# Optimization experiments

Measured on AMD Instinct MI355X. Metric: run time of the kernel, lower is better.

## Reference

```python
import jax, jax.numpy as jnp
import numpy as np

N = 50000       # nodes
E = 500000      # edges
F_IN = 64       # input feature dim
F_OUT = 64      # hidden/output dim
K = 3           # diffusion filter order
C = F_IN + F_OUT  # concat dim seen by each DConv


def _xavier(k, shape):
    fan_in, fan_out = shape[-2], shape[-1]
    lim = float(np.sqrt(6.0 / (fan_in + fan_out)))
    return jax.random.uniform(k, shape, jnp.float32, -lim, lim)


def setup_inputs() -> dict:
    key = jax.random.key(0)
    ks = jax.random.split(key, 8)
    X = jax.random.normal(ks[0], (N, F_IN), jnp.float32)
    H = jax.random.normal(ks[1], (N, F_OUT), jnp.float32)
    # ring edges guarantee every node has in-degree >= 1 and out-degree >= 1
    base = jnp.arange(N, dtype=jnp.int32)
    row = jnp.concatenate([base, jax.random.randint(ks[2], (E - N,), 0, N, jnp.int32)])
    col = jnp.concatenate([jnp.roll(base, 1), jax.random.randint(ks[3], (E - N,), 0, N, jnp.int32)])
    edge_index = jnp.stack([row, col])  # [2, E]
    W_z = _xavier(ks[4], (2, K, C, F_OUT))
    W_r = _xavier(ks[5], (2, K, C, F_OUT))
    W_h = _xavier(ks[6], (2, K, C, F_OUT))
    b = jnp.zeros((F_OUT,), jnp.float32)
    return {"X": X, "edge_index": edge_index, "H": H,
            "W_z": W_z, "b_z": b, "W_r": W_r, "b_r": b, "W_h": W_h, "b_h": b}


def _dconv(Xc, row, col, norm_out, norm_in, W, b):
    # PyG propagate: gather source (row) features, scale by edge norm, scatter-add to target (col)
    def prop(x, norm):
        return jax.ops.segment_sum(norm[:, None] * x[row], col, num_segments=N)
    Tx_0 = Xc
    Hout = Xc @ (W[0, 0] + W[1, 0])
    Tx_1_o = prop(Xc, norm_out)
    Tx_1_i = prop(Xc, norm_in)
    Hout = Hout + Tx_1_o @ W[0, 1] + Tx_1_i @ W[1, 1]
    for k in range(2, K):
        Tx_2_o = 2.0 * prop(Tx_1_o, norm_out) - Tx_0
        Tx_2_i = 2.0 * prop(Tx_1_i, norm_in) - Tx_0
        Hout = Hout + Tx_2_o @ W[0, k] + Tx_2_i @ W[1, k]
        # faithful to original: Tx_1 is never reassigned, so Tx_0 stays Xc
        Tx_0, Tx_1_o, Tx_1_i = Xc, Tx_2_o, Tx_2_i
    return Hout + b


def reference(X, edge_index, H, W_z, b_z, W_r, b_r, W_h, b_h):
    row, col = edge_index[0], edge_index[1]
    deg_out = jnp.zeros((N,), jnp.float32).at[row].add(1.0)
    deg_in = jnp.zeros((N,), jnp.float32).at[col].add(1.0)
    norm_out = (1.0 / deg_out)[row]
    norm_in = (1.0 / deg_in)[row]
    XH = jnp.concatenate([X, H], axis=1)
    Z = jax.nn.sigmoid(_dconv(XH, row, col, norm_out, norm_in, W_z, b_z))
    R = jax.nn.sigmoid(_dconv(XH, row, col, norm_out, norm_in, W_r, b_r))
    XHR = jnp.concatenate([X, H * R], axis=1)
    H_tilde = jnp.tanh(_dconv(XHR, row, col, norm_out, norm_in, W_h, b_h))
    H_new = Z * H + (1.0 - Z) * H_tilde
    # NaN infill with mean of non-NaN entries (faithful to original)
    mask = jnp.isnan(H_new)
    H_new = jnp.where(mask, jnp.nanmean(H_new), H_new)
    return H_new
```

## Files before the change

kernel.cpp:

```cpp
#include <hip/hip_runtime.h>
#include <hip/hip_bf16.h>
#include <math.h>

#define N_NODES 50000
#define N_EDGES 500000
#define C_DIM 128

typedef __attribute__((ext_vector_type(8))) short bf8;
typedef __attribute__((ext_vector_type(4))) float f32x4;

__device__ __forceinline__ float bflo(unsigned u) { return __uint_as_float(u << 16); }
__device__ __forceinline__ float bfhi(unsigned u) { return __uint_as_float(u & 0xffff0000u); }
__device__ __forceinline__ unsigned short f2bfu(float f) {
    __hip_bfloat16 h = __float2bfloat16(f);
    unsigned short u;
    __builtin_memcpy(&u, &h, 2);
    return u;
}
__device__ __forceinline__ unsigned packbf(float a, float b) {
    return ((unsigned)f2bfu(b) << 16) | f2bfu(a);
}


__global__ void count_deg(const int* __restrict__ row, const int* __restrict__ col,
                          int* __restrict__ dout, int* __restrict__ din, int e) {
    int i = blockIdx.x * blockDim.x + threadIdx.x;
    if (i >= e) return;
    atomicAdd(&dout[row[i]], 1);
    atomicAdd(&din[col[i]], 1);
}

__global__ void scan_block(const int* __restrict__ counts, int* __restrict__ excl,
                           int* __restrict__ blocksums, int n) {
    __shared__ int tmp[1024];
    int tid = threadIdx.x;
    int gid = blockIdx.x * 1024 + tid;
    int v = (gid < n) ? counts[gid] : 0;
    tmp[tid] = v;
    __syncthreads();
    for (int off = 1; off < 1024; off <<= 1) {
        int t = (tid >= off) ? tmp[tid - off] : 0;
        __syncthreads();
        tmp[tid] += t;
        __syncthreads();
    }
    int incl = tmp[tid];
    if (gid < n) excl[gid] = incl - v;
    if (tid == 1023) blocksums[blockIdx.x] = incl;
}

__global__ void scan_sums(int* __restrict__ blocksums, int nb) {
    __shared__ int tmp[64];
    int tid = threadIdx.x;
    int v = (tid < nb) ? blocksums[tid] : 0;
    tmp[tid] = v;
    __syncthreads();
    for (int off = 1; off < 64; off <<= 1) {
        int t = (tid >= off) ? tmp[tid - off] : 0;
        __syncthreads();
        tmp[tid] += t;
        __syncthreads();
    }
    if (tid < nb) blocksums[tid] = tmp[tid] - v;
}

__global__ void scan_add(int* __restrict__ rowptr, const int* __restrict__ blocksums,
                         int* __restrict__ cursor, const int* __restrict__ dout,
                         const int* __restrict__ din, float2* __restrict__ winv,
                         int n, int e_total) {
    int gid = blockIdx.x * blockDim.x + threadIdx.x;
    if (gid < n) {
        int v = rowptr[gid] + blocksums[gid >> 10];
        rowptr[gid] = v;
        cursor[gid] = v;
        winv[gid] = make_float2(1.0f / (float)dout[gid], 1.0f / (float)din[gid]);
    }
    if (gid == n) rowptr[n] = e_total;
}

__global__ void build_csr(const int* __restrict__ row, const int* __restrict__ col,
                          const float2* __restrict__ winv,
                          int* __restrict__ cursor, int* __restrict__ src,
                          float2* __restrict__ w, int e) {
    int i = blockIdx.x * blockDim.x + threadIdx.x;
    if (i >= e) return;
    int r = row[i], c = col[i];
    int pos = atomicAdd(&cursor[c], 1);
    src[pos] = r;
    w[pos] = winv[r];
}

__device__ __forceinline__ float wraw(const float* W, int d, int kk, int k, int j) {
    return W[((d * 3 + kk) * 128 + k) * 64 + j];
}

__global__ void pack_weights(const float* __restrict__ Wz, const float* __restrict__ Wr,
                             const float* __restrict__ Wh,
                             unsigned short* __restrict__ Wzr_t,
                             unsigned short* __restrict__ Wh_t) {
    int i = blockIdx.x * blockDim.x + threadIdx.x;
    if (i < 128 * 640) {
        int k = i % 640;
        int nn = i / 640;
        const float* W = (nn < 64) ? Wz : Wr;
        int j = nn & 63;
        float v;
        if (k < 128) {
            v = wraw(W, 0, 0, k, j) + wraw(W, 1, 0, k, j);
        } else {
            int k2 = k - 128;
            int kk = (k2 >= 256) ? 2 : 1;
            int k3 = k2 & 255;
            int p = k3 >> 2, sub = k3 & 3;
            v = wraw(W, sub >> 1, kk, 2 * p + (sub & 1), j);
        }
        Wzr_t[i] = f2bfu(v);
    } else if (i < 128 * 640 + 64 * 640) {
        int i2 = i - 128 * 640;
        int k = i2 % 640;
        int j = i2 / 640;
        float v;
        if (k < 64) {
            v = wraw(Wh, 0, 0, k, j) + wraw(Wh, 1, 0, k, j);
        } else if (k < 320) {
            int k2 = k - 64;
            int kk = (k2 >= 128) ? 2 : 1;
            int k3 = k2 & 127;
            int p = k3 >> 2, sub = k3 & 3;
            v = wraw(Wh, sub >> 1, kk, 2 * p + (sub & 1), j);
        } else if (k < 384) {
            int rr = k - 320;
            v = wraw(Wh, 0, 0, 64 + rr, j) + wraw(Wh, 1, 0, 64 + rr, j);
        } else {
            int k2 = k - 384;
            int kk = (k2 >= 128) ? 2 : 1;
            int k3 = k2 & 127;
            int p = k3 >> 2, sub = k3 & 3;
            v = wraw(Wh, sub >> 1, kk, 64 + 2 * p + (sub & 1), j);
        }
        Wh_t[i2] = f2bfu(v);
    }
}


__global__ void concat_xh(const float* __restrict__ X, const float* __restrict__ H,
                          unsigned short* __restrict__ XH, int n) {
    int i = blockIdx.x * blockDim.x + threadIdx.x;
    if (i >= n * C_DIM) return;
    int r = i >> 7, c = i & 127;
    float v = (c < 64) ? X[r * 64 + c] : H[r * 64 + (c - 64)];
    XH[i] = f2bfu(v);
}


__global__ void prop1_128(const unsigned short* __restrict__ S,
                          const int* __restrict__ rowptr, const int* __restrict__ src,
                          const float2* __restrict__ w,
                          unsigned short* __restrict__ P1, int n) {
    int tid = blockIdx.x * blockDim.x + threadIdx.x;
    int lane = tid & 63;
    int node = ((tid >> 6) << 1) + (lane >> 5);
    int p = lane & 31;
    if (node >= n) return;
    int beg = rowptr[node], end = rowptr[node + 1];
    float ao0 = 0.f, ao1 = 0.f, ao2 = 0.f, ao3 = 0.f;
    float ai0 = 0.f, ai1 = 0.f, ai2 = 0.f, ai3 = 0.f;
    int j = beg;
#define P1STEP(s_, w_) {                                                     \
        uint2 u = *(const uint2*)(S + (size_t)(s_) * 128 + 4 * p);           \
        float c0 = bflo(u.x), c1 = bfhi(u.x), c2 = bflo(u.y), c3 = bfhi(u.y);\
        ao0 = fmaf(w_.x, c0, ao0); ao1 = fmaf(w_.x, c1, ao1);                \
        ao2 = fmaf(w_.x, c2, ao2); ao3 = fmaf(w_.x, c3, ao3);                \
        ai0 = fmaf(w_.y, c0, ai0); ai1 = fmaf(w_.y, c1, ai1);                \
        ai2 = fmaf(w_.y, c2, ai2); ai3 = fmaf(w_.y, c3, ai3); }
    for (; j + 4 <= end; j += 4) {
        int s0 = src[j], s1 = src[j + 1], s2 = src[j + 2], s3 = src[j + 3];
        float2 w0 = w[j], w1 = w[j + 1], w2 = w[j + 2], w3 = w[j + 3];
        P1STEP(s0, w0); P1STEP(s1, w1); P1STEP(s2, w2); P1STEP(s3, w3);
    }
    for (; j < end; ++j) {
        int s = src[j]; float2 wv = w[j];
        P1STEP(s, wv);
    }
#undef P1STEP
    uint4 o;
    o.x = packbf(ao0, ao1); o.y = packbf(ai0, ai1);
    o.z = packbf(ao2, ao3); o.w = packbf(ai2, ai3);
    *(uint4*)(P1 + (size_t)node * 256 + 8 * p) = o;
}

__global__ void prop2_128(const unsigned short* __restrict__ P1,
                          const unsigned short* __restrict__ Xc,
                          const int* __restrict__ rowptr, const int* __restrict__ src,
                          const float2* __restrict__ w,
                          unsigned short* __restrict__ P2, int n) {
    int tid = blockIdx.x * blockDim.x + threadIdx.x;
    int lane = tid & 63;
    int node = ((tid >> 6) << 1) + (lane >> 5);
    int p = lane & 31;
    if (node >= n) return;
    int beg = rowptr[node], end = rowptr[node + 1];
    float oa = 0.f, ob = 0.f, oc = 0.f, od = 0.f;
    float ia = 0.f, ib = 0.f, ic = 0.f, id = 0.f;
    int j = beg;
#define P2STEP(s_, w_) {                                                     \
        uint4 v = *(const uint4*)(P1 + (size_t)(s_) * 256 + 8 * p);          \
        oa = fmaf(w_.x, bflo(v.x), oa); ob = fmaf(w_.x, bfhi(v.x), ob);      \
        ia = fmaf(w_.y, bflo(v.y), ia); ib = fmaf(w_.y, bfhi(v.y), ib);      \
        oc = fmaf(w_.x, bflo(v.z), oc); od = fmaf(w_.x, bfhi(v.z), od);      \
        ic = fmaf(w_.y, bflo(v.w), ic); id = fmaf(w_.y, bfhi(v.w), id); }
    for (; j + 4 <= end; j += 4) {
        int s0 = src[j], s1 = src[j + 1], s2 = src[j + 2], s3 = src[j + 3];
        float2 w0 = w[j], w1 = w[j + 1], w2 = w[j + 2], w3 = w[j + 3];
        P2STEP(s0, w0); P2STEP(s1, w1); P2STEP(s2, w2); P2STEP(s3, w3);
    }
    for (; j < end; ++j) {
        int s = src[j]; float2 wv = w[j];
        P2STEP(s, wv);
    }
#undef P2STEP
    uint2 ux = *(const uint2*)(Xc + (size_t)node * 128 + 4 * p);
    float xa = bflo(ux.x), xb = bfhi(ux.x), xc = bflo(ux.y), xd = bfhi(ux.y);
    uint4 o;
    o.x = packbf(2.f * oa - xa, 2.f * ob - xb);
    o.y = packbf(2.f * ia - xa, 2.f * ib - xb);
    o.z = packbf(2.f * oc - xc, 2.f * od - xd);
    o.w = packbf(2.f * ic - xc, 2.f * id - xd);
    *(uint4*)(P2 + (size_t)node * 256 + 8 * p) = o;
}

__global__ void prop1_64(const unsigned short* __restrict__ HR,
                         const int* __restrict__ rowptr, const int* __restrict__ src,
                         const float2* __restrict__ w,
                         unsigned short* __restrict__ Q1, int n) {
    int tid = blockIdx.x * blockDim.x + threadIdx.x;
    int lane = tid & 63;
    int node = ((tid >> 6) << 2) + (lane >> 4);
    int p = lane & 15;
    if (node >= n) return;
    int beg = rowptr[node], end = rowptr[node + 1];
    float ao0 = 0.f, ao1 = 0.f, ao2 = 0.f, ao3 = 0.f;
    float ai0 = 0.f, ai1 = 0.f, ai2 = 0.f, ai3 = 0.f;
    int j = beg;
#define Q1STEP(s_, w_) {                                                     \
        uint2 u = *(const uint2*)(HR + (size_t)(s_) * 64 + 4 * p);           \
        float c0 = bflo(u.x), c1 = bfhi(u.x), c2 = bflo(u.y), c3 = bfhi(u.y);\
        ao0 = fmaf(w_.x, c0, ao0); ao1 = fmaf(w_.x, c1, ao1);                \
        ao2 = fmaf(w_.x, c2, ao2); ao3 = fmaf(w_.x, c3, ao3);                \
        ai0 = fmaf(w_.y, c0, ai0); ai1 = fmaf(w_.y, c1, ai1);                \
        ai2 = fmaf(w_.y, c2, ai2); ai3 = fmaf(w_.y, c3, ai3); }
    for (; j + 4 <= end; j += 4) {
        int s0 = src[j], s1 = src[j + 1], s2 = src[j + 2], s3 = src[j + 3];
        float2 w0 = w[j], w1 = w[j + 1], w2 = w[j + 2], w3 = w[j + 3];
        Q1STEP(s0, w0); Q1STEP(s1, w1); Q1STEP(s2, w2); Q1STEP(s3, w3);
    }
    for (; j < end; ++j) {
        int s = src[j]; float2 wv = w[j];
        Q1STEP(s, wv);
    }
#undef Q1STEP
    uint4 o;
    o.x = packbf(ao0, ao1); o.y = packbf(ai0, ai1);
    o.z = packbf(ao2, ao3); o.w = packbf(ai2, ai3);
    *(uint4*)(Q1 + (size_t)node * 128 + 8 * p) = o;
}

__global__ void prop2_64(const unsigned short* __restrict__ Q1,
                         const unsigned short* __restrict__ HR,
                         const int* __restrict__ rowptr, const int* __restrict__ src,
                         const float2* __restrict__ w,
                         unsigned short* __restrict__ Q2, int n) {
    int tid = blockIdx.x * blockDim.x + threadIdx.x;
    int lane = tid & 63;
    int node = ((tid >> 6) << 2) + (lane >> 4);
    int p = lane & 15;
    if (node >= n) return;
    int beg = rowptr[node], end = rowptr[node + 1];
    float oa = 0.f, ob = 0.f, oc = 0.f, od = 0.f;
    float ia = 0.f, ib = 0.f, ic = 0.f, id = 0.f;
    int j = beg;
#define Q2STEP(s_, w_) {                                                     \
        uint4 v = *(const uint4*)(Q1 + (size_t)(s_) * 128 + 8 * p);          \
        oa = fmaf(w_.x, bflo(v.x), oa); ob = fmaf(w_.x, bfhi(v.x), ob);      \
        ia = fmaf(w_.y, bflo(v.y), ia); ib = fmaf(w_.y, bfhi(v.y), ib);      \
        oc = fmaf(w_.x, bflo(v.z), oc); od = fmaf(w_.x, bfhi(v.z), od);      \
        ic = fmaf(w_.y, bflo(v.w), ic); id = fmaf(w_.y, bfhi(v.w), id); }
    for (; j + 4 <= end; j += 4) {
        int s0 = src[j], s1 = src[j + 1], s2 = src[j + 2], s3 = src[j + 3];
        float2 w0 = w[j], w1 = w[j + 1], w2 = w[j + 2], w3 = w[j + 3];
        Q2STEP(s0, w0); Q2STEP(s1, w1); Q2STEP(s2, w2); Q2STEP(s3, w3);
    }
    for (; j < end; ++j) {
        int s = src[j]; float2 wv = w[j];
        Q2STEP(s, wv);
    }
#undef Q2STEP
    uint2 ux = *(const uint2*)(HR + (size_t)node * 64 + 4 * p);
    float xa = bflo(ux.x), xb = bfhi(ux.x), xc = bflo(ux.y), xd = bfhi(ux.y);
    uint4 o;
    o.x = packbf(2.f * oa - xa, 2.f * ob - xb);
    o.y = packbf(2.f * ia - xa, 2.f * ib - xb);
    o.z = packbf(2.f * oc - xc, 2.f * od - xd);
    o.w = packbf(2.f * ic - xc, 2.f * id - xd);
    *(uint4*)(Q2 + (size_t)node * 128 + 8 * p) = o;
}


__global__ __launch_bounds__(256) void gemm_zr_mfma(
    const unsigned short* __restrict__ XH, const unsigned short* __restrict__ P1,
    const unsigned short* __restrict__ P2,
    const unsigned short* __restrict__ Wt, const float* __restrict__ bz,
    const float* __restrict__ br, const float* __restrict__ H,
    float* __restrict__ Zf, unsigned short* __restrict__ HR, int n) {
    __shared__ uint2 Wl[128 * 66];
    int tid = threadIdx.x;
    int lane = tid & 63;
    int wid = tid >> 6;
    int mhalf = wid & 1, nhalf = wid >> 1;
    int rowbase = blockIdx.x * 64 + mhalf * 32;
    int lr = lane & 15, quad = lane >> 4;
    int r0 = rowbase + lr;       if (r0 >= n) r0 = n - 1;
    int r1 = rowbase + 16 + lr;  if (r1 >= n) r1 = n - 1;

    f32x4 zero = {0.f, 0.f, 0.f, 0.f};
    f32x4 acc[2][4];
#pragma unroll
    for (int a = 0; a < 2; ++a)
#pragma unroll
        for (int b = 0; b < 4; ++b) acc[a][b] = zero;

    const unsigned short* Ab[5] = {XH, P1, P1, P2, P2};
    const int Astr[5] = {128, 256, 256, 256, 256};
    const int Aoff[5] = {0, 0, 128, 0, 128};

    for (int c = 0; c < 5; ++c) {
        const unsigned short* Wsrc = Wt + c * 128;
        for (int i = tid; i < 128 * 16; i += 256) {
            int nrow = i >> 4, kp = i & 15;
            uint4 v = *(const uint4*)(Wsrc + (size_t)nrow * 640 + kp * 8);
            *(uint4*)&Wl[nrow * 66 + kp * 2] = v;
        }
        __syncthreads();
        const unsigned short* A0 = Ab[c] + (size_t)r0 * Astr[c] + Aoff[c] + quad * 8;
        const unsigned short* A1 = Ab[c] + (size_t)r1 * Astr[c] + Aoff[c] + quad * 8;
#pragma unroll
        for (int kk = 0; kk < 4; ++kk) {
            bf8 a0 = *(const bf8*)(A0 + kk * 32);
            bf8 a1 = *(const bf8*)(A1 + kk * 32);
#pragma unroll
            for (int nt = 0; nt < 4; ++nt) {
                int nrow = nhalf * 64 + nt * 16 + lr;
                int base = nrow * 66 + kk * 8 + quad * 2;
                union { bf8 v; uint2 h[2]; } bb;
                bb.h[0] = Wl[base];
                bb.h[1] = Wl[base + 1];
                acc[0][nt] = __builtin_amdgcn_mfma_f32_16x16x32_bf16(a0, bb.v, acc[0][nt], 0, 0, 0);
                acc[1][nt] = __builtin_amdgcn_mfma_f32_16x16x32_bf16(a1, bb.v, acc[1][nt], 0, 0, 0);
            }
        }
        __syncthreads();
    }
#pragma unroll
    for (int mt = 0; mt < 2; ++mt)
#pragma unroll
        for (int reg = 0; reg < 4; ++reg) {
            int r = rowbase + mt * 16 + quad * 4 + reg;
            if (r >= n) continue;
#pragma unroll
            for (int nt = 0; nt < 4; ++nt) {
                int cidx = nhalf * 64 + nt * 16 + lr;
                float bias = (cidx < 64) ? bz[cidx] : br[cidx - 64];
                float v = acc[mt][nt][reg] + bias;
                float s = 1.f / (1.f + expf(-v));
                if (cidx < 64) {
                    Zf[(size_t)r * 64 + cidx] = s;
                } else {
                    int c2 = cidx - 64;
                    HR[(size_t)r * 64 + c2] = f2bfu(H[(size_t)r * 64 + c2] * s);
                }
            }
        }
}

__global__ __launch_bounds__(256) void gemm_h_mfma(
    const unsigned short* __restrict__ XH, const unsigned short* __restrict__ P1,
    const unsigned short* __restrict__ P2, const unsigned short* __restrict__ HR,
    const unsigned short* __restrict__ Q1, const unsigned short* __restrict__ Q2,
    const unsigned short* __restrict__ Wt, const float* __restrict__ bh,
    const float* __restrict__ Zf, const float* __restrict__ H,
    float* __restrict__ out, int n) {
    __shared__ uint2 Wl[64 * 66];
    int tid = threadIdx.x;
    int lane = tid & 63;
    int wid = tid >> 6;
    int mhalf = wid & 1, nhalf = wid >> 1;
    int rowbase = blockIdx.x * 64 + mhalf * 32;
    int lr = lane & 15, quad = lane >> 4;
    int r0 = rowbase + lr;       if (r0 >= n) r0 = n - 1;
    int r1 = rowbase + 16 + lr;  if (r1 >= n) r1 = n - 1;

    f32x4 zero = {0.f, 0.f, 0.f, 0.f};
    f32x4 acc[2][2];
#pragma unroll
    for (int a = 0; a < 2; ++a)
#pragma unroll
        for (int b = 0; b < 2; ++b) acc[a][b] = zero;

    const unsigned short* Ab[6] = {XH, P1, P2, HR, Q1, Q2};
    const int Astr[6] = {128, 256, 256, 64, 128, 128};
    const int Aklen[6] = {64, 128, 128, 64, 128, 128};
    const int Akg[6] = {0, 64, 192, 320, 384, 512};

    for (int sg = 0; sg < 6; ++sg) {
        int klen = Aklen[sg];
        int units = 64 * (klen >> 3);
        const unsigned short* Wsrc = Wt + Akg[sg];
        for (int i = tid; i < units; i += 256) {
            int kcnt = klen >> 3;
            int nrow = i / kcnt, kp = i % kcnt;
            uint4 v = *(const uint4*)(Wsrc + (size_t)nrow * 640 + kp * 8);
            *(uint4*)&Wl[nrow * 66 + kp * 2] = v;
        }
        __syncthreads();
        const unsigned short* A0 = Ab[sg] + (size_t)r0 * Astr[sg] + quad * 8;
        const unsigned short* A1 = Ab[sg] + (size_t)r1 * Astr[sg] + quad * 8;
        int nkk = klen >> 5;
        for (int kk = 0; kk < nkk; ++kk) {
            bf8 a0 = *(const bf8*)(A0 + kk * 32);
            bf8 a1 = *(const bf8*)(A1 + kk * 32);
#pragma unroll
            for (int nt = 0; nt < 2; ++nt) {
                int nrow = nhalf * 32 + nt * 16 + lr;
                int base = nrow * 66 + kk * 8 + quad * 2;
                union { bf8 v; uint2 h[2]; } bb;
                bb.h[0] = Wl[base];
                bb.h[1] = Wl[base + 1];
                acc[0][nt] = __builtin_amdgcn_mfma_f32_16x16x32_bf16(a0, bb.v, acc[0][nt], 0, 0, 0);
                acc[1][nt] = __builtin_amdgcn_mfma_f32_16x16x32_bf16(a1, bb.v, acc[1][nt], 0, 0, 0);
            }
        }
        __syncthreads();
    }
#pragma unroll
    for (int mt = 0; mt < 2; ++mt)
#pragma unroll
        for (int reg = 0; reg < 4; ++reg) {
            int r = rowbase + mt * 16 + quad * 4 + reg;
            if (r >= n) continue;
#pragma unroll
            for (int nt = 0; nt < 2; ++nt) {
                int cidx = nhalf * 32 + nt * 16 + lr;
                float ht = tanhf(acc[mt][nt][reg] + bh[cidx]);
                float z = Zf[(size_t)r * 64 + cidx];
                float h_old = H[(size_t)r * 64 + cidx];
                out[(size_t)r * 64 + cidx] = z * h_old + (1.f - z) * ht;
            }
        }
}


static inline size_t rup(size_t x) { return (x + 63) & ~(size_t)63; }

extern "C" void kernel_launch(void* const* d_in, const int* in_sizes, int n_in,
                              void* d_out, int out_size, void* d_ws, size_t ws_size,
                              hipStream_t stream) {
    const float* X  = (const float*)d_in[0];
    const int*   EI = (const int*)d_in[1];
    const float* H  = (const float*)d_in[2];
    const float* Wz = (const float*)d_in[3];
    const float* bz = (const float*)d_in[4];
    const float* Wr = (const float*)d_in[5];
    const float* br = (const float*)d_in[6];
    const float* Wh = (const float*)d_in[7];
    const float* bh = (const float*)d_in[8];
    float* out = (float*)d_out;

    const int* row = EI;
    const int* col = EI + N_EDGES;

    char* ws = (char*)d_ws;
    size_t off = 0;
    auto carve = [&](size_t bytes) { void* p = ws + off; off += rup(bytes); return p; };

    int*   deg_out   = (int*)carve(N_NODES * 4);
    int*   deg_in    = (int*)carve(N_NODES * 4);
    int*   rowptr    = (int*)carve((N_NODES + 1) * 4);
    int*   cursor    = (int*)carve(N_NODES * 4);
    int*   blocksums = (int*)carve(64 * 4);
    float2* winv     = (float2*)carve(N_NODES * 8);
    int*   csr_src   = (int*)carve(N_EDGES * 4);
    float2* csr_w    = (float2*)carve(N_EDGES * 8);
    unsigned short* XH = (unsigned short*)carve((size_t)N_NODES * 128 * 2);
    unsigned short* P1 = (unsigned short*)carve((size_t)N_NODES * 256 * 2);
    unsigned short* P2 = (unsigned short*)carve((size_t)N_NODES * 256 * 2);
    unsigned short* HR = (unsigned short*)carve((size_t)N_NODES * 64 * 2);
    unsigned short* Q1 = (unsigned short*)carve((size_t)N_NODES * 128 * 2);
    unsigned short* Q2 = (unsigned short*)carve((size_t)N_NODES * 128 * 2);
    float* Zf          = (float*)carve((size_t)N_NODES * 64 * 4);
    unsigned short* Wzr_t = (unsigned short*)carve(128 * 640 * 2);
    unsigned short* Wh_t  = (unsigned short*)carve(64 * 640 * 2);

    hipMemsetAsync(deg_out, 0, rup(N_NODES * 4) + rup(N_NODES * 4), stream);
    count_deg<<<(N_EDGES + 255) / 256, 256, 0, stream>>>(row, col, deg_out, deg_in, N_EDGES);

    int nblk = (N_NODES + 1023) / 1024;
    scan_block<<<nblk, 1024, 0, stream>>>(deg_in, rowptr, blocksums, N_NODES);
    scan_sums<<<1, 64, 0, stream>>>(blocksums, nblk);
    scan_add<<<(N_NODES + 1 + 255) / 256, 256, 0, stream>>>(rowptr, blocksums, cursor,
                                                            deg_out, deg_in, winv, N_NODES, N_EDGES);

    build_csr<<<(N_EDGES + 255) / 256, 256, 0, stream>>>(row, col, winv, cursor,
                                                         csr_src, csr_w, N_EDGES);

    pack_weights<<<(128 * 640 + 64 * 640 + 255) / 256, 256, 0, stream>>>(Wz, Wr, Wh, Wzr_t, Wh_t);

    concat_xh<<<(N_NODES * C_DIM + 255) / 256, 256, 0, stream>>>(X, H, XH, N_NODES);

    int blocks_p128 = (((N_NODES + 1) / 2) * 64 + 255) / 256;
    prop1_128<<<blocks_p128, 256, 0, stream>>>(XH, rowptr, csr_src, csr_w, P1, N_NODES);
    prop2_128<<<blocks_p128, 256, 0, stream>>>(P1, XH, rowptr, csr_src, csr_w, P2, N_NODES);

    int gemm_blocks = (N_NODES + 63) / 64;
    gemm_zr_mfma<<<gemm_blocks, 256, 0, stream>>>(XH, P1, P2, Wzr_t, bz, br, H, Zf, HR, N_NODES);

    int blocks_p64 = (((N_NODES + 3) / 4) * 64 + 255) / 256;
    prop1_64<<<blocks_p64, 256, 0, stream>>>(HR, rowptr, csr_src, csr_w, Q1, N_NODES);
    prop2_64<<<blocks_p64, 256, 0, stream>>>(Q1, HR, rowptr, csr_src, csr_w, Q2, N_NODES);

    gemm_h_mfma<<<gemm_blocks, 256, 0, stream>>>(XH, P1, P2, HR, Q1, Q2,
                                                 Wh_t, bh, Zf, H, out, N_NODES);
}
```

Before: 393.0 us.

## Load GEMM weight fragments directly into registers, drop LDS staging and barriers

Both MFMA GEMM kernels stop staging weight chunks in shared memory with __syncthreads between K segments. Each wave now loads its B fragments straight from global (L2-cached) memory into a 20-entry register array per K half, then runs the MFMAs over the A rows. In the ZR kernel the wave tiling also changes, so each wave covers all 64 rows and 32 output columns. This removes LDS traffic and block barriers, at the cost of more VGPR pressure and redundant weight loads from global memory per block.

```diff
diff --git a/kernel.cpp b/kernel.cpp
--- a/kernel.cpp
+++ b/kernel.cpp
@@ -312,63 +312,68 @@
     const unsigned short* __restrict__ Wt, const float* __restrict__ bz,
     const float* __restrict__ br, const float* __restrict__ H,
     float* __restrict__ Zf, unsigned short* __restrict__ HR, int n) {
-    __shared__ uint2 Wl[128 * 66];
     int tid = threadIdx.x;
     int lane = tid & 63;
-    int wid = tid >> 6;
-    int mhalf = wid & 1, nhalf = wid >> 1;
-    int rowbase = blockIdx.x * 64 + mhalf * 32;
+    int ngrp = tid >> 6;
+    int rowbase = blockIdx.x * 64;
     int lr = lane & 15, quad = lane >> 4;
-    int r0 = rowbase + lr;       if (r0 >= n) r0 = n - 1;
-    int r1 = rowbase + 16 + lr;  if (r1 >= n) r1 = n - 1;
+
+    const unsigned short* A0[4];
+    const unsigned short* A1[4];
+    const unsigned short* A2[4];
+#pragma unroll
+    for (int mt = 0; mt < 4; ++mt) {
+        int r = rowbase + mt * 16 + lr;
+        if (r >= n) r = n - 1;
+        A0[mt] = XH + (size_t)r * 128 + quad * 8;
+        A1[mt] = P1 + (size_t)r * 256 + quad * 8;
+        A2[mt] = P2 + (size_t)r * 256 + quad * 8;
+    }
+    const unsigned short* Wb = Wt + (size_t)(ngrp * 32 + lr) * 640 + quad * 8;
 
     f32x4 zero = {0.f, 0.f, 0.f, 0.f};
-    f32x4 acc[2][4];
-#pragma unroll
-    for (int a = 0; a < 2; ++a)
-#pragma unroll
-        for (int b = 0; b < 4; ++b) acc[a][b] = zero;
-
-    const unsigned short* Ab[5] = {XH, P1, P1, P2, P2};
-    const int Astr[5] = {128, 256, 256, 256, 256};
-    const int Aoff[5] = {0, 0, 128, 0, 128};
-
-    for (int c = 0; c < 5; ++c) {
-        const unsigned short* Wsrc = Wt + c * 128;
-        for (int i = tid; i < 128 * 16; i += 256) {
-            int nrow = i >> 4, kp = i & 15;
-            uint4 v = *(const uint4*)(Wsrc + (size_t)nrow * 640 + kp * 8);
-            *(uint4*)&Wl[nrow * 66 + kp * 2] = v;
-        }
-        __syncthreads();
-        const unsigned short* A0 = Ab[c] + (size_t)r0 * Astr[c] + Aoff[c] + quad * 8;
-        const unsigned short* A1 = Ab[c] + (size_t)r1 * Astr[c] + Aoff[c] + quad * 8;
-#pragma unroll
-        for (int kk = 0; kk < 4; ++kk) {
-            bf8 a0 = *(const bf8*)(A0 + kk * 32);
-            bf8 a1 = *(const bf8*)(A1 + kk * 32);
-#pragma unroll
-            for (int nt = 0; nt < 4; ++nt) {
-                int nrow = nhalf * 64 + nt * 16 + lr;
-                int base = nrow * 66 + kk * 8 + quad * 2;
-                union { bf8 v; uint2 h[2]; } bb;
-                bb.h[0] = Wl[base];
-                bb.h[1] = Wl[base + 1];
-                acc[0][nt] = __builtin_amdgcn_mfma_f32_16x16x32_bf16(a0, bb.v, acc[0][nt], 0, 0, 0);
-                acc[1][nt] = __builtin_amdgcn_mfma_f32_16x16x32_bf16(a1, bb.v, acc[1][nt], 0, 0, 0);
+    f32x4 acc[4][2];
+#pragma unroll
+    for (int a = 0; a < 4; ++a)
+#pragma unroll
+        for (int b = 0; b < 2; ++b) acc[a][b] = zero;
+
+#pragma unroll
+    for (int kh = 0; kh < 2; ++kh) {
+        bf8 Breg[20];
+#pragma unroll
+        for (int kl = 0; kl < 10; ++kl) {
+            int ks = kh * 10 + kl;
+#pragma unroll
+            for (int nt = 0; nt < 2; ++nt)
+                Breg[kl * 2 + nt] = *(const bf8*)(Wb + (size_t)nt * 16 * 640 + ks * 32);
+        }
+#pragma unroll
+        for (int kl = 0; kl < 10; ++kl) {
+            int ks = kh * 10 + kl;
+#pragma unroll
+            for (int mt = 0; mt < 4; ++mt) {
+                const unsigned short* ap =
+                    (ks < 4)  ? (A0[mt] + ks * 32) :
+                    (ks < 12) ? (A1[mt] + (ks - 4) * 32) :
+                                (A2[mt] + (ks - 12) * 32);
+                bf8 a = *(const bf8*)ap;
+#pragma unroll
+                for (int nt = 0; nt < 2; ++nt)
+                    acc[mt][nt] = __builtin_amdgcn_mfma_f32_16x16x32_bf16(
+                        a, Breg[kl * 2 + nt], acc[mt][nt], 0, 0, 0);
             }
         }
-        __syncthreads();
-    }
-#pragma unroll
-    for (int mt = 0; mt < 2; ++mt)
+    }
+#pragma unroll
+    for (int mt = 0; mt < 4; ++mt)
 #pragma unroll
         for (int reg = 0; reg < 4; ++reg) {
             int r = rowbase + mt * 16 + quad * 4 + reg;
             if (r >= n) continue;
 #pragma unroll
-            for (int nt = 0; nt < 4; ++nt) {
-                int cidx = nhalf * 64 + nt * 16 + lr;
+            for (int nt = 0; nt < 2; ++nt) {
+                int cidx = ngrp * 32 + nt * 16 + lr;
                 float bias = (cidx < 64) ? bz[cidx] : br[cidx - 64];
                 float v = acc[mt][nt][reg] + bias;
                 float s = 1.f / (1.f + expf(-v));
@@ -389,15 +394,31 @@
     const unsigned short* __restrict__ Wt, const float* __restrict__ bh,
     const float* __restrict__ Zf, const float* __restrict__ H,
     float* __restrict__ out, int n) {
-    __shared__ uint2 Wl[64 * 66];
     int tid = threadIdx.x;
     int lane = tid & 63;
     int wid = tid >> 6;
-    int mhalf = wid & 1, nhalf = wid >> 1;
+    int mhalf = wid & 1, ngrp = wid >> 1;
     int rowbase = blockIdx.x * 64 + mhalf * 32;
     int lr = lane & 15, quad = lane >> 4;
-    int r0 = rowbase + lr;       if (r0 >= n) r0 = n - 1;
-    int r1 = rowbase + 16 + lr;  if (r1 >= n) r1 = n - 1;
+
+    const unsigned short* S0[2];
+    const unsigned short* S1[2];
+    const unsigned short* S2[2];
+    const unsigned short* S3[2];
+    const unsigned short* S4[2];
+    const unsigned short* S5[2];
+#pragma unroll
+    for (int mt = 0; mt < 2; ++mt) {
+        int r = rowbase + mt * 16 + lr;
+        if (r >= n) r = n - 1;
+        S0[mt] = XH + (size_t)r * 128 + quad * 8;
+        S1[mt] = P1 + (size_t)r * 256 + quad * 8;
+        S2[mt] = P2 + (size_t)r * 256 + quad * 8;
+        S3[mt] = HR + (size_t)r * 64 + quad * 8;
+        S4[mt] = Q1 + (size_t)r * 128 + quad * 8;
+        S5[mt] = Q2 + (size_t)r * 128 + quad * 8;
+    }
+    const unsigned short* Wb = Wt + (size_t)(ngrp * 32 + lr) * 640 + quad * 8;
 
     f32x4 zero = {0.f, 0.f, 0.f, 0.f};
     f32x4 acc[2][2];
@@ -406,40 +427,35 @@
 #pragma unroll
         for (int b = 0; b < 2; ++b) acc[a][b] = zero;
 
-    const unsigned short* Ab[6] = {XH, P1, P2, HR, Q1, Q2};
-    const int Astr[6] = {128, 256, 256, 64, 128, 128};
-    const int Aklen[6] = {64, 128, 128, 64, 128, 128};
-    const int Akg[6] = {0, 64, 192, 320, 384, 512};
-
-    for (int sg = 0; sg < 6; ++sg) {
-        int klen = Aklen[sg];
-        int units = 64 * (klen >> 3);
-        const unsigned short* Wsrc = Wt + Akg[sg];
-        for (int i = tid; i < units; i += 256) {
-            int kcnt = klen >> 3;
-            int nrow = i / kcnt, kp = i % kcnt;
-            uint4 v = *(const uint4*)(Wsrc + (size_t)nrow * 640 + kp * 8);
-            *(uint4*)&Wl[nrow * 66 + kp * 2] = v;
-        }
-        __syncthreads();
-        const unsigned short* A0 = Ab[sg] + (size_t)r0 * Astr[sg] + quad * 8;
-        const unsigned short* A1 = Ab[sg] + (size_t)r1 * Astr[sg] + quad * 8;
-        int nkk = klen >> 5;
-        for (int kk = 0; kk < nkk; ++kk) {
-            bf8 a0 = *(const bf8*)(A0 + kk * 32);
-            bf8 a1 = *(const bf8*)(A1 + kk * 32);
-#pragma unroll
-            for (int nt = 0; nt < 2; ++nt) {
-                int nrow = nhalf * 32 + nt * 16 + lr;
-                int base = nrow * 66 + kk * 8 + quad * 2;
-                union { bf8 v; uint2 h[2]; } bb;
-                bb.h[0] = Wl[base];
-                bb.h[1] = Wl[base + 1];
-                acc[0][nt] = __builtin_amdgcn_mfma_f32_16x16x32_bf16(a0, bb.v, acc[0][nt], 0, 0, 0);
-                acc[1][nt] = __builtin_amdgcn_mfma_f32_16x16x32_bf16(a1, bb.v, acc[1][nt], 0, 0, 0);
+#pragma unroll
+    for (int kh = 0; kh < 2; ++kh) {
+        bf8 Breg[20];
+#pragma unroll
+        for (int kl = 0; kl < 10; ++kl) {
+            int ks = kh * 10 + kl;
+#pragma unroll
+            for (int nt = 0; nt < 2; ++nt)
+                Breg[kl * 2 + nt] = *(const bf8*)(Wb + (size_t)nt * 16 * 640 + ks * 32);
+        }
+#pragma unroll
+        for (int kl = 0; kl < 10; ++kl) {
+            int ks = kh * 10 + kl;
+#pragma unroll
+            for (int mt = 0; mt < 2; ++mt) {
+                const unsigned short* ap =
+                    (ks < 2)  ? (S0[mt] + ks * 32) :
+                    (ks < 6)  ? (S1[mt] + (ks - 2) * 32) :
+                    (ks < 10) ? (S2[mt] + (ks - 6) * 32) :
+                    (ks < 12) ? (S3[mt] + (ks - 10) * 32) :
+                    (ks < 16) ? (S4[mt] + (ks - 12) * 32) :
+                                (S5[mt] + (ks - 16) * 32);
+                bf8 a = *(const bf8*)ap;
+#pragma unroll
+                for (int nt = 0; nt < 2; ++nt)
+                    acc[mt][nt] = __builtin_amdgcn_mfma_f32_16x16x32_bf16(
+                        a, Breg[kl * 2 + nt], acc[mt][nt], 0, 0, 0);
             }
         }
-        __syncthreads();
     }
 #pragma unroll
     for (int mt = 0; mt < 2; ++mt)
@@ -449,7 +465,7 @@
             if (r >= n) continue;
 #pragma unroll
             for (int nt = 0; nt < 2; ++nt) {
-                int cidx = nhalf * 32 + nt * 16 + lr;
+                int cidx = ngrp * 32 + nt * 16 + lr;
                 float ht = tanhf(acc[mt][nt][reg] + bh[cidx]);
                 float z = Zf[(size_t)r * 64 + cidx];
                 float h_old = H[(size_t)r * 64 + cidx];
```

Measured after the change: 409.7 us. 1.04x slower.

## Double-buffer GEMM A/B tiles in LDS via async global_load_lds

Applied to the files above, without the earlier changes.

Both MFMA GEMM kernels now stage A and weight tiles into LDS in 64-wide K chunks using the direct global-to-LDS load builtin, with two buffers so the next chunk loads while the current one is multiplied. A is no longer read straight from global memory into registers per wave, so each A tile is shared across waves. This aims to hide global latency and cut redundant A loads. The cost is more LDS use, per-chunk barriers and a fixed 10-chunk loop. Unpadded LDS layouts may cause bank conflicts, and there is no explicit vmcnt wait beyond the barrier.

```diff
diff --git a/kernel.cpp b/kernel.cpp
--- a/kernel.cpp
+++ b/kernel.cpp
@@ -19,6 +19,12 @@
 }
 __device__ __forceinline__ unsigned packbf(float a, float b) {
     return ((unsigned)f2bfu(b) << 16) | f2bfu(a);
+}
+
+__device__ __forceinline__ void gload_lds16(const void* g, void* l) {
+    __builtin_amdgcn_global_load_lds(
+        (const __attribute__((address_space(1))) void*)g,
+        (__attribute__((address_space(3))) void*)l, 16, 0, 0);
 }
 
 
@@ -312,15 +318,39 @@
     const unsigned short* __restrict__ Wt, const float* __restrict__ bz,
     const float* __restrict__ br, const float* __restrict__ H,
     float* __restrict__ Zf, unsigned short* __restrict__ HR, int n) {
-    __shared__ uint2 Wl[128 * 66];
+    __shared__ unsigned short Al[2][8 * 64 * 8];
+    __shared__ unsigned short Bl[2][8 * 128 * 8];
     int tid = threadIdx.x;
     int lane = tid & 63;
     int wid = tid >> 6;
-    int mhalf = wid & 1, nhalf = wid >> 1;
-    int rowbase = blockIdx.x * 64 + mhalf * 32;
+    int mh = wid & 1, nh = wid >> 1;
+    int rowbase = blockIdx.x * 64;
     int lr = lane & 15, quad = lane >> 4;
-    int r0 = rowbase + lr;       if (r0 >= n) r0 = n - 1;
-    int r1 = rowbase + 16 + lr;  if (r1 >= n) r1 = n - 1;
+
+    auto stage = [&](int c, int buf) {
+        const unsigned short* T;
+        int str, toff;
+        if (c < 2)      { T = XH; str = 128; toff = c * 64; }
+        else if (c < 6) { T = P1; str = 256; toff = (c - 2) * 64; }
+        else            { T = P2; str = 256; toff = (c - 6) * 64; }
+        int kb = c * 64;
+        int grow = rowbase + lane; if (grow >= n) grow = n - 1;
+#pragma unroll
+        for (int j = 0; j < 6; ++j) {
+            int idx = wid * 6 + j;
+            if (idx < 8) {
+                int q = idx;
+                gload_lds16(T + (size_t)grow * str + toff + q * 8,
+                            &Al[buf][q * 512]);
+            } else {
+                int t = idx - 8;
+                int q = t >> 1, h = t & 1;
+                int col = h * 64 + lane;
+                gload_lds16(Wt + (size_t)col * 640 + kb + q * 8,
+                            &Bl[buf][q * 1024 + h * 512]);
+            }
+        }
+    };
 
     f32x4 zero = {0.f, 0.f, 0.f, 0.f};
     f32x4 acc[2][4];
@@ -329,46 +359,38 @@
 #pragma unroll
         for (int b = 0; b < 4; ++b) acc[a][b] = zero;
 
-    const unsigned short* Ab[5] = {XH, P1, P1, P2, P2};
-    const int Astr[5] = {128, 256, 256, 256, 256};
-    const int Aoff[5] = {0, 0, 128, 0, 128};
-
-    for (int c = 0; c < 5; ++c) {
-        const unsigned short* Wsrc = Wt + c * 128;
-        for (int i = tid; i < 128 * 16; i += 256) {
-            int nrow = i >> 4, kp = i & 15;
-            uint4 v = *(const uint4*)(Wsrc + (size_t)nrow * 640 + kp * 8);
-            *(uint4*)&Wl[nrow * 66 + kp * 2] = v;
-        }
+    stage(0, 0);
+    for (int c = 0; c < 10; ++c) {
+        int buf = c & 1;
         __syncthreads();
-        const unsigned short* A0 = Ab[c] + (size_t)r0 * Astr[c] + Aoff[c] + quad * 8;
-        const unsigned short* A1 = Ab[c] + (size_t)r1 * Astr[c] + Aoff[c] + quad * 8;
-#pragma unroll
-        for (int kk = 0; kk < 4; ++kk) {
-            bf8 a0 = *(const bf8*)(A0 + kk * 32);
-            bf8 a1 = *(const bf8*)(A1 + kk * 32);
+        if (c < 9) stage(c + 1, buf ^ 1);
+#pragma unroll
+        for (int s = 0; s < 2; ++s) {
+            int q = s * 4 + quad;
+            bf8 af[2], bfr[4];
+#pragma unroll
+            for (int mt = 0; mt < 2; ++mt)
+                af[mt] = *(const bf8*)&Al[buf][q * 512 + (mh * 32 + mt * 16 + lr) * 8];
+#pragma unroll
+            for (int nt = 0; nt < 4; ++nt)
+                bfr[nt] = *(const bf8*)&Bl[buf][q * 1024 + (nh * 64 + nt * 16 + lr) * 8];
+#pragma unroll
+            for (int mt = 0; mt < 2; ++mt)
+#pragma unroll
+                for (int nt = 0; nt < 4; ++nt)
+                    acc[mt][nt] = __builtin_amdgcn_mfma_f32_16x16x32_bf16(
+                        af[mt], bfr[nt], acc[mt][nt], 0, 0, 0);
+        }
+    }
+#pragma unroll
+    for (int mt = 0; mt < 2; ++mt)
+#pragma unroll
+        for (int reg = 0; reg < 4; ++reg) {
+            int r = rowbase + mh * 32 + mt * 16 + quad * 4 + reg;
+            if (r >= n) continue;
 #pragma unroll
             for (int nt = 0; nt < 4; ++nt) {
-                int nrow = nhalf * 64 + nt * 16 + lr;
-                int base = nrow * 66 + kk * 8 + quad * 2;
-                union { bf8 v; uint2 h[2]; } bb;
-                bb.h[0] = Wl[base];
-                bb.h[1] = Wl[base + 1];
-                acc[0][nt] = __builtin_amdgcn_mfma_f32_16x16x32_bf16(a0, bb.v, acc[0][nt], 0, 0, 0);
-                acc[1][nt] = __builtin_amdgcn_mfma_f32_16x16x32_bf16(a1, bb.v, acc[1][nt], 0, 0, 0);
-            }
-        }
-        __syncthreads();
-    }
-#pragma unroll
-    for (int mt = 0; mt < 2; ++mt)
-#pragma unroll
-        for (int reg = 0; reg < 4; ++reg) {
-            int r = rowbase + mt * 16 + quad * 4 + reg;
-            if (r >= n) continue;
-#pragma unroll
-            for (int nt = 0; nt < 4; ++nt) {
-                int cidx = nhalf * 64 + nt * 16 + lr;
+                int cidx = nh * 64 + nt * 16 + lr;
                 float bias = (cidx < 64) ? bz[cidx] : br[cidx - 64];
                 float v = acc[mt][nt][reg] + bias;
                 float s = 1.f / (1.f + expf(-v));
@@ -389,15 +411,40 @@
     const unsigned short* __restrict__ Wt, const float* __restrict__ bh,
     const float* __restrict__ Zf, const float* __restrict__ H,
     float* __restrict__ out, int n) {
-    __shared__ uint2 Wl[64 * 66];
+    __shared__ unsigned short Al[2][8 * 64 * 8];
+    __shared__ unsigned short Bl[2][8 * 64 * 8];
     int tid = threadIdx.x;
     int lane = tid & 63;
     int wid = tid >> 6;
-    int mhalf = wid & 1, nhalf = wid >> 1;
-    int rowbase = blockIdx.x * 64 + mhalf * 32;
+    int mh = wid & 1, nh = wid >> 1;
+    int rowbase = blockIdx.x * 64;
     int lr = lane & 15, quad = lane >> 4;
-    int r0 = rowbase + lr;       if (r0 >= n) r0 = n - 1;
-    int r1 = rowbase + 16 + lr;  if (r1 >= n) r1 = n - 1;
+
+    auto stage = [&](int c, int buf) {
+        const unsigned short* T;
+        int str, toff;
+        if (c == 0)      { T = XH; str = 128; toff = 0; }
+        else if (c < 3)  { T = P1; str = 256; toff = (c - 1) * 64; }
+        else if (c < 5)  { T = P2; str = 256; toff = (c - 3) * 64; }
+        else if (c == 5) { T = HR; str = 64;  toff = 0; }
+        else if (c < 8)  { T = Q1; str = 128; toff = (c - 6) * 64; }
+        else             { T = Q2; str = 128; toff = (c - 8) * 64; }
+        int kb = c * 64;
+        int grow = rowbase + lane; if (grow >= n) grow = n - 1;
+#pragma unroll
+        for (int j = 0; j < 4; ++j) {
+            int idx = wid * 4 + j;
+            if (idx < 8) {
+                int q = idx;
+                gload_lds16(T + (size_t)grow * str + toff + q * 8,
+                            &Al[buf][q * 512]);
+            } else {
+                int q = idx - 8;
+                gload_lds16(Wt + (size_t)lane * 640 + kb + q * 8,
+                            &Bl[buf][q * 512]);
+            }
+        }
+    };
 
     f32x4 zero = {0.f, 0.f, 0.f, 0.f};
     f32x4 acc[2][2];
@@ -406,50 +453,38 @@
 #pragma unroll
         for (int b = 0; b < 2; ++b) acc[a][b] = zero;
 
-    const unsigned short* Ab[6] = {XH, P1, P2, HR, Q1, Q2};
-    const int Astr[6] = {128, 256, 256, 64, 128, 128};
-    const int Aklen[6] = {64, 128, 128, 64, 128, 128};
-    const int Akg[6] = {0, 64, 192, 320, 384, 512};
-
-    for (int sg = 0; sg < 6; ++sg) {
-        int klen = Aklen[sg];
-        int units = 64 * (klen >> 3);
-        const unsigned short* Wsrc = Wt + Akg[sg];
-        for (int i = tid; i < units; i += 256) {
-            int kcnt = klen >> 3;
-            int nrow = i / kcnt, kp = i % kcnt;
-            uint4 v = *(const uint4*)(Wsrc + (size_t)nrow * 640 + kp * 8);
-            *(uint4*)&Wl[nrow * 66 + kp * 2] = v;
-        }
+    stage(0, 0);
+    for (int c = 0; c < 10; ++c) {
+        int buf = c & 1;
         __syncthreads();
-        const unsigned short* A0 = Ab[sg] + (size_t)r0 * Astr[sg] + quad * 8;
-        const unsigned short* A1 = Ab[sg] + (size_t)r1 * Astr[sg] + quad * 8;
-        int nkk = klen >> 5;
-        for (int kk = 0; kk < nkk; ++kk) {
-            bf8 a0 = *(const bf8*)(A0 + kk * 32);
-            bf8 a1 = *(const bf8*)(A1 + kk * 32);
+        if (c < 9) stage(c + 1, buf ^ 1);
+#pragma unroll
+        for (int s = 0; s < 2; ++s) {
+            int q = s * 4 + quad;
+            bf8 af[2], bfr[2];
+#pragma unroll
+            for (int mt = 0; mt < 2; ++mt)
+                af[mt] = *(const bf8*)&Al[buf][q * 512 + (mh * 32 + mt * 16 + lr) * 8];
+#pragma unroll
+            for (int nt = 0; nt < 2; ++nt)
+                bfr[nt] = *(const bf8*)&Bl[buf][q * 512 + (nh * 32 + nt * 16 + lr) * 8];
+#pragma unroll
+            for (int mt = 0; mt < 2; ++mt)
+#pragma unroll
+                for (int nt = 0; nt < 2; ++nt)
+                    acc[mt][nt] = __builtin_amdgcn_mfma_f32_16x16x32_bf16(
+                        af[mt], bfr[nt], acc[mt][nt], 0, 0, 0);
+        }
+    }
+#pragma unroll
+    for (int mt = 0; mt < 2; ++mt)
+#pragma unroll
+        for (int reg = 0; reg < 4; ++reg) {
+            int r = rowbase + mh * 32 + mt * 16 + quad * 4 + reg;
+            if (r >= n) continue;
 #pragma unroll
             for (int nt = 0; nt < 2; ++nt) {
-                int nrow = nhalf * 32 + nt * 16 + lr;
-                int base = nrow * 66 + kk * 8 + quad * 2;
-                union { bf8 v; uint2 h[2]; } bb;
-                bb.h[0] = Wl[base];
-                bb.h[1] = Wl[base + 1];
-                acc[0][nt] = __builtin_amdgcn_mfma_f32_16x16x32_bf16(a0, bb.v, acc[0][nt], 0, 0, 0);
-                acc[1][nt] = __builtin_amdgcn_mfma_f32_16x16x32_bf16(a1, bb.v, acc[1][nt], 0, 0, 0);
-            }
-        }
-        __syncthreads();
-    }
-#pragma unroll
-    for (int mt = 0; mt < 2; ++mt)
-#pragma unroll
-        for (int reg = 0; reg < 4; ++reg) {
-            int r = rowbase + mt * 16 + quad * 4 + reg;
-            if (r >= n) continue;
-#pragma unroll
-            for (int nt = 0; nt < 2; ++nt) {
-                int cidx = nhalf * 32 + nt * 16 + lr;
+                int cidx = nh * 32 + nt * 16 + lr;
                 float ht = tanhf(acc[mt][nt][reg] + bh[cidx]);
                 float z = Zf[(size_t)r * 64 + cidx];
                 float h_old = H[(size_t)r * 64 + cidx];
```

Measured after the change: 407.7 us. +3.7%, slower.
